# Kernel tuning notes

Hardware: AMD Instinct MI355X
Metric: run time of the kernel (lower is better)

Reference implementation:

```python
import jax, jax.numpy as jnp
import numpy as np

N_NODES = 50000
N_EDGES = 500000
D_IN, D_HID = 128, 256


def _add_self_loops(edge_index, n):
    loop = jnp.arange(n, dtype=edge_index.dtype)
    src = jnp.concatenate([edge_index[0], loop])
    dst = jnp.concatenate([edge_index[1], loop])
    return src, dst


def _gcn_layer(x, W, b, src, dst, dinv_sqrt, n):
    # x: [N, d_in] -> h: [N, d_out]
    h = x @ W
    # symmetric normalization D^{-1/2} (A+I) D^{-1/2}
    norm = dinv_sqrt[src] * dinv_sqrt[dst]          # [E+N]
    msg = h[src] * norm[:, None]                    # gather + scale
    agg = jax.ops.segment_sum(msg, dst, num_segments=n)  # scatter-add
    return agg + b


def setup_inputs() -> dict:
    key = jax.random.key(0)
    ks = jax.random.split(key, 8)
    x = jax.random.normal(ks[0], (N_NODES, D_IN), dtype=jnp.float32)
    edge_index = jax.random.randint(ks[1], (2, N_EDGES), 0, N_NODES, dtype=jnp.int64 if jax.config.read('jax_enable_x64') else jnp.int32)
    s = lambda fan_in: 1.0 / np.sqrt(fan_in)
    W1 = jax.random.uniform(ks[2], (D_IN, D_HID), jnp.float32, -s(D_IN), s(D_IN))
    b1 = jnp.zeros((D_HID,), jnp.float32)
    W2 = jax.random.uniform(ks[3], (D_HID, D_HID), jnp.float32, -s(D_HID), s(D_HID))
    b2 = jnp.zeros((D_HID,), jnp.float32)
    W3 = jax.random.uniform(ks[4], (D_HID, D_HID), jnp.float32, -s(D_HID), s(D_HID))
    b3 = jnp.zeros((D_HID,), jnp.float32)
    return {"x": x, "edge_index": edge_index, "W1": W1, "b1": b1,
            "W2": W2, "b2": b2, "W3": W3, "b3": b3}


def reference(x, edge_index, W1, b1, W2, b2, W3, b3):
    n = x.shape[0]
    src, dst = _add_self_loops(edge_index, n)
    # degree includes self loops (edge weight 1), as in torch_geometric GCNConv
    deg = jax.ops.segment_sum(jnp.ones_like(dst, dtype=x.dtype), dst, num_segments=n)
    dinv_sqrt = jnp.where(deg > 0, jax.lax.rsqrt(jnp.maximum(deg, 1e-12)), 0.0)
    h = jax.nn.relu(_gcn_layer(x, W1, b1, src, dst, dinv_sqrt, n))
    h = jax.nn.relu(_gcn_layer(h, W2, b2, src, dst, dinv_sqrt, n))
    h = _gcn_layer(h, W3, b3, src, dst, dinv_sqrt, n)
    return h
```

## Files before the change

### kernel.cpp

```cpp
#include <hip/hip_runtime.h>

#define NNODES 50000
#define NEDGES 500000
#define DIN 128
#define DHID 256
#define MPAD 50048
#define NI4 12500
#define NSB 49

typedef unsigned short u16;
typedef __attribute__((ext_vector_type(8))) _Float16 half8;
typedef __attribute__((ext_vector_type(4))) float f32x4;

__device__ __forceinline__ u16 f2h(float f) {
  union { _Float16 h; u16 u; } v; v.h = (_Float16)f; return v.u;
}
__device__ __forceinline__ float h2f(unsigned int u) {
  union { _Float16 h; u16 u; } v; v.u = (u16)u; return (float)v.h;
}

__global__ void k_zero_i32(int* __restrict__ p, int n) {
  int i = blockIdx.x * blockDim.x + threadIdx.x;
  if (i < n) p[i] = 0;
}

__global__ void k_hist(const int* __restrict__ dst, int* __restrict__ deg, int e) {
  int i = blockIdx.x * blockDim.x + threadIdx.x;
  if (i < e) atomicAdd(&deg[dst[i]], 1);
}

__global__ __launch_bounds__(256) void k_blocksum(const int* __restrict__ deg,
                                                  int* __restrict__ partials) {
  __shared__ int red[256];
  int tid = threadIdx.x;
  int t4 = blockIdx.x * 256 + tid;
  int sum = 0;
  if (t4 < NI4) {
    int4 v = ((const int4*)deg)[t4];
    sum = v.x + v.y + v.z + v.w;
  }
  red[tid] = sum;
  __syncthreads();
  for (int off = 128; off > 0; off >>= 1) {
    if (tid < off) red[tid] += red[tid + off];
    __syncthreads();
  }
  if (tid == 0) partials[blockIdx.x] = red[0];
}

__global__ __launch_bounds__(256) void k_scan2(int* __restrict__ deg,
                                               const int* __restrict__ partials,
                                               int* __restrict__ row_ptr,
                                               float* __restrict__ dinv) {
  __shared__ int sdata[256];
  __shared__ int sprefix;
  int tid = threadIdx.x, bid = blockIdx.x;
  int t4 = bid * 256 + tid;
  int4 v = make_int4(0, 0, 0, 0);
  if (t4 < NI4) v = ((const int4*)deg)[t4];
  int tsum = v.x + v.y + v.z + v.w;
  sdata[tid] = tsum;
  if (tid == 0) {
    int pre = 0;
    for (int b = 0; b < bid; ++b) pre += partials[b];
    sprefix = pre;
  }
  __syncthreads();
  for (int off = 1; off < 256; off <<= 1) {
    int val = (tid >= off) ? sdata[tid - off] : 0;
    __syncthreads();
    sdata[tid] += val;
    __syncthreads();
  }
  if (t4 < NI4) {
    int run = sdata[tid] - tsum + sprefix;
    int base = t4 * 4;
    float4 dv;
    dv.x = rsqrtf((float)v.x + 1.0f);
    dv.y = rsqrtf((float)v.y + 1.0f);
    dv.z = rsqrtf((float)v.z + 1.0f);
    dv.w = rsqrtf((float)v.w + 1.0f);
    *(float4*)(dinv + base) = dv;
    row_ptr[base + 0] = run; run += v.x;
    row_ptr[base + 1] = run; run += v.y;
    row_ptr[base + 2] = run; run += v.z;
    row_ptr[base + 3] = run; run += v.w;
    if (base + 4 == NNODES) row_ptr[NNODES] = run;
    ((int4*)deg)[t4] = make_int4(0, 0, 0, 0);
  }
}

__global__ void k_fill(const int* __restrict__ src, const int* __restrict__ dst,
                       const float* __restrict__ dinv, const int* __restrict__ row_ptr,
                       int* __restrict__ cursor, int* __restrict__ csr_src,
                       float* __restrict__ csr_nrm, int e) {
  int i = blockIdx.x * blockDim.x + threadIdx.x;
  if (i < e) {
    int d = dst[i], s = src[i];
    int pos = row_ptr[d] + atomicAdd(&cursor[d], 1);
    csr_src[pos] = s;
    csr_nrm[pos] = dinv[s] * dinv[d];
  }
}

__global__ void k_prep(const float* __restrict__ x, u16* __restrict__ xh, int total4,
                       const float* __restrict__ W1f, u16* __restrict__ P1,
                       const float* __restrict__ W2f, u16* __restrict__ P2,
                       const float* __restrict__ W3f, u16* __restrict__ P3) {
  int i = blockIdx.x * blockDim.x + threadIdx.x;
  if (i < total4) {
    float4 v = ((const float4*)x)[i];
    ushort4 o;
    o.x = f2h(v.x); o.y = f2h(v.y); o.z = f2h(v.z); o.w = f2h(v.w);
    ((ushort4*)xh)[i] = o;
  }
  const int s1 = DIN * 256, s2 = s1 + DHID * 256, s3 = s2 + DHID * 256;
  if (i < s3) {
    const float* W; u16* P; int li;
    if (i < s1)      { W = W1f; P = P1; li = i; }
    else if (i < s2) { W = W2f; P = P2; li = i - s1; }
    else             { W = W3f; P = P3; li = i - s2; }
    int k = li >> 8, n = li & 255;
    int t = k >> 5, q = (k >> 3) & 3, j = k & 7;
    int c = n >> 4, m = n & 15;
    int f = (c * 64 + q * 16 + m) * 8 + j;
    float w = W[li] * 256.0f;
    u16 hi = f2h(w);
    u16 lo = f2h(w - h2f(hi));
    P[(size_t)t * 16384 + f] = hi;
    P[(size_t)t * 16384 + 8192 + f] = lo;
  }
}

template<int K, int EPI>
__global__ __launch_bounds__(256, 6) void k_fused(const u16* __restrict__ hf,
                                                  const float* __restrict__ dinv,
                                                  const int* __restrict__ row_ptr,
                                                  const int* __restrict__ csr_src,
                                                  const float* __restrict__ csr_nrm,
                                                  const u16* __restrict__ Bpk,
                                                  const float* __restrict__ bias,
                                                  u16* __restrict__ hf16,
                                                  float* __restrict__ outf) {
  __shared__ __align__(16) u16 As[32 * K];
  __shared__ int nextrow;

  const int lane = threadIdx.x & 63;
  const int wave = threadIdx.x >> 6;

  if (threadIdx.x == 0) nextrow = 0;
  __syncthreads();

  {
    constexpr int GL = K / 8;
    const int sub = threadIdx.x % GL;
    const int gbase = lane - (lane % GL);
    const int coff = sub * 8;
    const int nbase = blockIdx.x * 32;

    for (;;) {
      int row;
      if (sub == 0) row = atomicAdd(&nextrow, 1);
      row = __shfl(row, gbase);
      if (row >= 32) break;
      const int node = nbase + row;
      float acc[8];
      if (node < NNODES) {
        float di = dinv[node];
        float s2 = di * di;
        {
          half8 v = *(const half8*)(hf + (size_t)node * K + coff);
#pragma unroll
          for (int j = 0; j < 8; ++j) acc[j] = s2 * (float)v[j];
        }
        const int p0 = row_ptr[node];
        const int p1 = row_ptr[node + 1];
        for (int e = p0; e < p1; e += 4) {
          int idx[4]; float w[4];
#pragma unroll
          for (int q = 0; q < 4; ++q) {
            int ii = (e + q < p1) ? e + q : p1 - 1;
            idx[q] = csr_src[ii];
            w[q] = (e + q < p1) ? csr_nrm[ii] : 0.0f;
          }
          half8 v[4];
#pragma unroll
          for (int q = 0; q < 4; ++q)
            v[q] = *(const half8*)(hf + (size_t)idx[q] * K + coff);
#pragma unroll
          for (int q = 0; q < 4; ++q)
#pragma unroll
            for (int j = 0; j < 8; ++j)
              acc[j] = fmaf(w[q], (float)v[q][j], acc[j]);
        }
      } else {
#pragma unroll
        for (int j = 0; j < 8; ++j) acc[j] = 0.0f;
      }
      const int wc = coff ^ ((row & 7) << 3);
      uint4 o;
      o.x = (unsigned)f2h(acc[0]) | ((unsigned)f2h(acc[1]) << 16);
      o.y = (unsigned)f2h(acc[2]) | ((unsigned)f2h(acc[3]) << 16);
      o.z = (unsigned)f2h(acc[4]) | ((unsigned)f2h(acc[5]) << 16);
      o.w = (unsigned)f2h(acc[6]) | ((unsigned)f2h(acc[7]) << 16);
      *(uint4*)&As[row * K + wc] = o;
    }
  }

  __syncthreads();

  const int cb = wave * 4;
  const int lr0 = lane & 15;
  const int lr1 = 16 + lr0;
  const int acoff = (lane >> 4) * 8;

  f32x4 acc0[4], acc1[4];
#pragma unroll
  for (int c = 0; c < 4; ++c) {
    acc0[c] = {0.f, 0.f, 0.f, 0.f};
    acc1[c] = {0.f, 0.f, 0.f, 0.f};
  }

  for (int t = 0; t < K / 32; ++t) {
    const int ac = acoff + t * 32;
    half8 a0 = *(const half8*)&As[lr0 * K + (ac ^ ((lr0 & 7) << 3))];
    half8 a1 = *(const half8*)&As[lr1 * K + (ac ^ ((lr1 & 7) << 3))];
    const u16* bt = Bpk + (size_t)t * 16384 + ((size_t)cb * 64 + lane) * 8;
#pragma unroll
    for (int c = 0; c < 4; ++c) {
      const u16* fb = bt + c * 512;
      half8 bh = *(const half8*)fb;
      half8 bl = *(const half8*)(fb + 8192);
      acc0[c] = __builtin_amdgcn_mfma_f32_16x16x32_f16(a0, bh, acc0[c], 0, 0, 0);
      acc0[c] = __builtin_amdgcn_mfma_f32_16x16x32_f16(a0, bl, acc0[c], 0, 0, 0);
      acc1[c] = __builtin_amdgcn_mfma_f32_16x16x32_f16(a1, bh, acc1[c], 0, 0, 0);
      acc1[c] = __builtin_amdgcn_mfma_f32_16x16x32_f16(a1, bl, acc1[c], 0, 0, 0);
    }
  }

  const int cbase = lane & 15;
  const int r0 = blockIdx.x * 32 + ((lane >> 4) * 4);
  const float sc = 1.0f / 256.0f;
#pragma unroll
  for (int c = 0; c < 4; ++c) {
    int col = (cb + c) * 16 + cbase;
    float bv = bias[col];
#pragma unroll
    for (int r = 0; r < 4; ++r) {
      float v0 = fmaf(acc0[c][r], sc, bv);
      float v1 = fmaf(acc1[c][r], sc, bv);
      if (EPI == 0) {
        v0 = fmaxf(v0, 0.f);
        v1 = fmaxf(v1, 0.f);
        hf16[(size_t)(r0 + r) * 256 + col] = f2h(v0);
        hf16[(size_t)(r0 + 16 + r) * 256 + col] = f2h(v1);
      } else {
        if (r0 + r < NNODES) outf[(size_t)(r0 + r) * 256 + col] = v0;
        if (r0 + 16 + r < NNODES) outf[(size_t)(r0 + 16 + r) * 256 + col] = v1;
      }
    }
  }
}

extern "C" void kernel_launch(void* const* d_in, const int* in_sizes, int n_in,
                              void* d_out, int out_size, void* d_ws, size_t ws_size,
                              hipStream_t stream) {
  const float* x  = (const float*)d_in[0];
  const int*   ei = (const int*)d_in[1];
  const float* W1 = (const float*)d_in[2];
  const float* b1 = (const float*)d_in[3];
  const float* W2 = (const float*)d_in[4];
  const float* b2 = (const float*)d_in[5];
  const float* W3 = (const float*)d_in[6];
  const float* b3 = (const float*)d_in[7];
  float* out = (float*)d_out;
  (void)in_sizes; (void)n_in; (void)out_size; (void)ws_size;

  char* ws = (char*)d_ws;
  size_t off = 0;
  auto alloc = [&](size_t bytes) -> void* {
    void* p = (void*)(ws + off);
    off += (bytes + 255) & ~(size_t)255;
    return p;
  };
  float* dinv    = (float*)alloc((size_t)NNODES * 4);
  int*   deg     = (int*)alloc((size_t)NNODES * 4);
  int*   row_ptr = (int*)alloc((size_t)(NNODES + 1) * 4);
  int*   partials= (int*)alloc((size_t)NSB * 4);
  int*   csr_src = (int*)alloc((size_t)NEDGES * 4);
  float* csr_nrm = (float*)alloc((size_t)NEDGES * 4);
  u16*   xh      = (u16*)alloc((size_t)NNODES * DIN * 2);
  u16*   hbufA   = (u16*)alloc((size_t)MPAD * 256 * 2);
  u16*   hbufB   = (u16*)alloc((size_t)MPAD * 256 * 2);
  u16*   W1pk    = (u16*)alloc((size_t)(DIN / 32) * 16384 * 2);
  u16*   W2pk    = (u16*)alloc((size_t)(DHID / 32) * 16384 * 2);
  u16*   W3pk    = (u16*)alloc((size_t)(DHID / 32) * 16384 * 2);

  const int* e_src = ei;
  const int* e_dst = ei + NEDGES;

  const int tb = 256;
  k_zero_i32<<<(NNODES + tb - 1) / tb, tb, 0, stream>>>(deg, NNODES);
  k_hist<<<(NEDGES + tb - 1) / tb, tb, 0, stream>>>(e_dst, deg, NEDGES);
  k_blocksum<<<NSB, 256, 0, stream>>>(deg, partials);
  k_scan2<<<NSB, 256, 0, stream>>>(deg, partials, row_ptr, dinv);
  k_fill<<<(NEDGES + tb - 1) / tb, tb, 0, stream>>>(e_src, e_dst, dinv, row_ptr, deg,
                                                    csr_src, csr_nrm, NEDGES);

  int x4 = NNODES * DIN / 4;
  k_prep<<<(x4 + tb - 1) / tb, tb, 0, stream>>>(x, xh, x4,
                                                W1, W1pk, W2, W2pk, W3, W3pk);

  const int gblocks = (NNODES + 31) / 32;

  k_fused<DIN, 0><<<gblocks, 256, 0, stream>>>(xh, dinv, row_ptr, csr_src, csr_nrm,
                                               W1pk, b1, hbufA, nullptr);
  k_fused<DHID, 0><<<gblocks, 256, 0, stream>>>(hbufA, dinv, row_ptr, csr_src, csr_nrm,
                                                W2pk, b2, hbufB, nullptr);
  k_fused<DHID, 1><<<gblocks, 256, 0, stream>>>(hbufB, dinv, row_ptr, csr_src, csr_nrm,
                                                W3pk, b3, nullptr, out);
}
```

Before: 305.8 us.

## Split fused GCN tile into two halves, overlapping gather with MFMA GEMM

Each 32-row block is split into two 16-row sub-tiles with separate LDS buffers. After the first half is gathered, odd waves gather the second half while even waves run the GEMM on the first half (and vice versa), so sparse gathers overlap MFMA work within a block. The zeroing kernel for degree counts is also folded into k_prep, which moves ahead of the histogram, removing one launch. The trade-off is that B fragments are loaded twice per block (once per 16-row tile) and there is an extra barrier.

```diff
diff --git a/kernel.cpp b/kernel.cpp
--- a/kernel.cpp
+++ b/kernel.cpp
@@ -17,11 +17,6 @@
 }
 __device__ __forceinline__ float h2f(unsigned int u) {
   union { _Float16 h; u16 u; } v; v.u = (u16)u; return (float)v.h;
-}
-
-__global__ void k_zero_i32(int* __restrict__ p, int n) {
-  int i = blockIdx.x * blockDim.x + threadIdx.x;
-  if (i < n) p[i] = 0;
 }
 
 __global__ void k_hist(const int* __restrict__ dst, int* __restrict__ deg, int e) {
@@ -104,10 +99,12 @@
 }
 
 __global__ void k_prep(const float* __restrict__ x, u16* __restrict__ xh, int total4,
+                       int* __restrict__ deg,
                        const float* __restrict__ W1f, u16* __restrict__ P1,
                        const float* __restrict__ W2f, u16* __restrict__ P2,
                        const float* __restrict__ W3f, u16* __restrict__ P3) {
   int i = blockIdx.x * blockDim.x + threadIdx.x;
+  if (i < NI4) ((int4*)deg)[i] = make_int4(0, 0, 0, 0);
   if (i < total4) {
     float4 v = ((const float4*)x)[i];
     ushort4 o;
@@ -142,28 +139,27 @@
                                                   const float* __restrict__ bias,
                                                   u16* __restrict__ hf16,
                                                   float* __restrict__ outf) {
-  __shared__ __align__(16) u16 As[32 * K];
-  __shared__ int nextrow;
+  __shared__ __align__(16) u16 As[2][16 * K];
+  __shared__ int nextrow[2];
 
   const int lane = threadIdx.x & 63;
   const int wave = threadIdx.x >> 6;
 
-  if (threadIdx.x == 0) nextrow = 0;
-  __syncthreads();
-
-  {
-    constexpr int GL = K / 8;
-    const int sub = threadIdx.x % GL;
-    const int gbase = lane - (lane % GL);
-    const int coff = sub * 8;
-    const int nbase = blockIdx.x * 32;
-
+  if (threadIdx.x < 2) nextrow[threadIdx.x] = 0;
+  __syncthreads();
+
+  constexpr int GL = K / 8;
+  const int sub = threadIdx.x % GL;
+  const int gbase = lane - (lane % GL);
+  const int coff = sub * 8;
+
+  auto gather_tile = [&](int tbase, int buf, int cidx) {
     for (;;) {
-      int row;
-      if (sub == 0) row = atomicAdd(&nextrow, 1);
+      int row = 0;
+      if (sub == 0) row = atomicAdd(&nextrow[cidx], 1);
       row = __shfl(row, gbase);
-      if (row >= 32) break;
-      const int node = nbase + row;
+      if (row >= 16) break;
+      const int node = tbase + row;
       float acc[8];
       if (node < NNODES) {
         float di = dinv[node];
@@ -203,63 +199,61 @@
       o.y = (unsigned)f2h(acc[2]) | ((unsigned)f2h(acc[3]) << 16);
       o.z = (unsigned)f2h(acc[4]) | ((unsigned)f2h(acc[5]) << 16);
       o.w = (unsigned)f2h(acc[6]) | ((unsigned)f2h(acc[7]) << 16);
-      *(uint4*)&As[row * K + wc] = o;
+      *(uint4*)&As[buf][row * K + wc] = o;
     }
-  }
-
-  __syncthreads();
-
-  const int cb = wave * 4;
-  const int lr0 = lane & 15;
-  const int lr1 = 16 + lr0;
-  const int acoff = (lane >> 4) * 8;
-
-  f32x4 acc0[4], acc1[4];
-#pragma unroll
-  for (int c = 0; c < 4; ++c) {
-    acc0[c] = {0.f, 0.f, 0.f, 0.f};
-    acc1[c] = {0.f, 0.f, 0.f, 0.f};
-  }
-
-  for (int t = 0; t < K / 32; ++t) {
-    const int ac = acoff + t * 32;
-    half8 a0 = *(const half8*)&As[lr0 * K + (ac ^ ((lr0 & 7) << 3))];
-    half8 a1 = *(const half8*)&As[lr1 * K + (ac ^ ((lr1 & 7) << 3))];
-    const u16* bt = Bpk + (size_t)t * 16384 + ((size_t)cb * 64 + lane) * 8;
-#pragma unroll
-    for (int c = 0; c < 4; ++c) {
-      const u16* fb = bt + c * 512;
-      half8 bh = *(const half8*)fb;
-      half8 bl = *(const half8*)(fb + 8192);
-      acc0[c] = __builtin_amdgcn_mfma_f32_16x16x32_f16(a0, bh, acc0[c], 0, 0, 0);
-      acc0[c] = __builtin_amdgcn_mfma_f32_16x16x32_f16(a0, bl, acc0[c], 0, 0, 0);
-      acc1[c] = __builtin_amdgcn_mfma_f32_16x16x32_f16(a1, bh, acc1[c], 0, 0, 0);
-      acc1[c] = __builtin_amdgcn_mfma_f32_16x16x32_f16(a1, bl, acc1[c], 0, 0, 0);
-    }
-  }
-
-  const int cbase = lane & 15;
-  const int r0 = blockIdx.x * 32 + ((lane >> 4) * 4);
-  const float sc = 1.0f / 256.0f;
-#pragma unroll
-  for (int c = 0; c < 4; ++c) {
-    int col = (cb + c) * 16 + cbase;
-    float bv = bias[col];
-#pragma unroll
-    for (int r = 0; r < 4; ++r) {
-      float v0 = fmaf(acc0[c][r], sc, bv);
-      float v1 = fmaf(acc1[c][r], sc, bv);
-      if (EPI == 0) {
-        v0 = fmaxf(v0, 0.f);
-        v1 = fmaxf(v1, 0.f);
-        hf16[(size_t)(r0 + r) * 256 + col] = f2h(v0);
-        hf16[(size_t)(r0 + 16 + r) * 256 + col] = f2h(v1);
-      } else {
-        if (r0 + r < NNODES) outf[(size_t)(r0 + r) * 256 + col] = v0;
-        if (r0 + 16 + r < NNODES) outf[(size_t)(r0 + 16 + r) * 256 + col] = v1;
+  };
+
+  auto gemm_tile = [&](int tbase, int buf) {
+    const int cb = wave * 4;
+    const int lr = lane & 15;
+    const int acoff = (lane >> 4) * 8;
+
+    f32x4 acc0[4];
+#pragma unroll
+    for (int c = 0; c < 4; ++c) acc0[c] = {0.f, 0.f, 0.f, 0.f};
+
+    for (int t = 0; t < K / 32; ++t) {
+      const int ac = acoff + t * 32;
+      half8 a0 = *(const half8*)&As[buf][lr * K + (ac ^ ((lr & 7) << 3))];
+      const u16* bt = Bpk + (size_t)t * 16384 + ((size_t)cb * 64 + lane) * 8;
+#pragma unroll
+      for (int c = 0; c < 4; ++c) {
+        const u16* fb = bt + c * 512;
+        half8 bh = *(const half8*)fb;
+        half8 bl = *(const half8*)(fb + 8192);
+        acc0[c] = __builtin_amdgcn_mfma_f32_16x16x32_f16(a0, bh, acc0[c], 0, 0, 0);
+        acc0[c] = __builtin_amdgcn_mfma_f32_16x16x32_f16(a0, bl, acc0[c], 0, 0, 0);
       }
     }
-  }
+
+    const int cbase = lane & 15;
+    const int r0 = tbase + ((lane >> 4) * 4);
+    const float sc = 1.0f / 256.0f;
+#pragma unroll
+    for (int c = 0; c < 4; ++c) {
+      int col = (cb + c) * 16 + cbase;
+      float bv = bias[col];
+#pragma unroll
+      for (int r = 0; r < 4; ++r) {
+        float v0 = fmaf(acc0[c][r], sc, bv);
+        if (EPI == 0) {
+          v0 = fmaxf(v0, 0.f);
+          hf16[(size_t)(r0 + r) * 256 + col] = f2h(v0);
+        } else {
+          if (r0 + r < NNODES) outf[(size_t)(r0 + r) * 256 + col] = v0;
+        }
+      }
+    }
+  };
+
+  const int b0 = blockIdx.x * 32;
+
+  gather_tile(b0, 0, 0);
+  __syncthreads();
+  if (wave & 1) { gather_tile(b0 + 16, 1, 1); gemm_tile(b0, 0); }
+  else          { gemm_tile(b0, 0); gather_tile(b0 + 16, 1, 1); }
+  __syncthreads();
+  gemm_tile(b0 + 16, 1);
 }
 
 extern "C" void kernel_launch(void* const* d_in, const int* in_sizes, int n_in,
@@ -300,16 +294,14 @@
   const int* e_dst = ei + NEDGES;
 
   const int tb = 256;
-  k_zero_i32<<<(NNODES + tb - 1) / tb, tb, 0, stream>>>(deg, NNODES);
+  int x4 = NNODES * DIN / 4;
+  k_prep<<<(x4 + tb - 1) / tb, tb, 0, stream>>>(x, xh, x4, deg,
+                                                W1, W1pk, W2, W2pk, W3, W3pk);
   k_hist<<<(NEDGES + tb - 1) / tb, tb, 0, stream>>>(e_dst, deg, NEDGES);
   k_blocksum<<<NSB, 256, 0, stream>>>(deg, partials);
   k_scan2<<<NSB, 256, 0, stream>>>(deg, partials, row_ptr, dinv);
   k_fill<<<(NEDGES + tb - 1) / tb, tb, 0, stream>>>(e_src, e_dst, dinv, row_ptr, deg,
                                                     csr_src, csr_nrm, NEDGES);
-
-  int x4 = NNODES * DIN / 4;
-  k_prep<<<(x4 + tb - 1) / tb, tb, 0, stream>>>(x, xh, x4,
-                                                W1, W1pk, W2, W2pk, W3, W3pk);
 
   const int gblocks = (NNODES + 31) / 32;
 
```

Measured after the change: 356.6 us. 16.6% more time.

## Merge graph preprocessing kernels into one cooperative kernel with grid syncs

Applied to the files above, without the earlier changes.

Replaces six separate preprocessing launches (zero, histogram, block sums, scan, CSR fill, fp16/weight packing) with a single cooperative kernel of 1024 blocks that uses grid.sync between phases. The goal is to remove per-launch overhead and let the x/weight conversion overlap with the degree zeroing. The cost is four grid-wide barriers, plus grid-stride loops over fewer threads, which may add serialization. Cooperative launch also requires all 1024 blocks to be co-resident.

```diff
diff --git a/kernel.cpp b/kernel.cpp
--- a/kernel.cpp
+++ b/kernel.cpp
@@ -1,4 +1,7 @@
 #include <hip/hip_runtime.h>
+#include <hip/hip_cooperative_groups.h>
+
+namespace cg = cooperative_groups;
 
 #define NNODES 50000
 #define NEDGES 500000
@@ -19,116 +22,116 @@
   union { _Float16 h; u16 u; } v; v.u = (u16)u; return (float)v.h;
 }
 
-__global__ void k_zero_i32(int* __restrict__ p, int n) {
-  int i = blockIdx.x * blockDim.x + threadIdx.x;
-  if (i < n) p[i] = 0;
-}
-
-__global__ void k_hist(const int* __restrict__ dst, int* __restrict__ deg, int e) {
-  int i = blockIdx.x * blockDim.x + threadIdx.x;
-  if (i < e) atomicAdd(&deg[dst[i]], 1);
-}
-
-__global__ __launch_bounds__(256) void k_blocksum(const int* __restrict__ deg,
-                                                  int* __restrict__ partials) {
-  __shared__ int red[256];
-  int tid = threadIdx.x;
-  int t4 = blockIdx.x * 256 + tid;
-  int sum = 0;
-  if (t4 < NI4) {
-    int4 v = ((const int4*)deg)[t4];
-    sum = v.x + v.y + v.z + v.w;
-  }
-  red[tid] = sum;
-  __syncthreads();
-  for (int off = 128; off > 0; off >>= 1) {
-    if (tid < off) red[tid] += red[tid + off];
-    __syncthreads();
-  }
-  if (tid == 0) partials[blockIdx.x] = red[0];
-}
-
-__global__ __launch_bounds__(256) void k_scan2(int* __restrict__ deg,
-                                               const int* __restrict__ partials,
-                                               int* __restrict__ row_ptr,
-                                               float* __restrict__ dinv) {
+__global__ __launch_bounds__(256, 4) void k_build(
+    const float* __restrict__ x, u16* __restrict__ xh, int total4,
+    int* __restrict__ deg,
+    const float* __restrict__ W1f, u16* __restrict__ P1,
+    const float* __restrict__ W2f, u16* __restrict__ P2,
+    const float* __restrict__ W3f, u16* __restrict__ P3,
+    const int* __restrict__ esrc, const int* __restrict__ edst,
+    int* __restrict__ row_ptr, float* __restrict__ dinv,
+    int* __restrict__ partials, int* __restrict__ csr_src,
+    float* __restrict__ csr_nrm) {
+  cg::grid_group grid = cg::this_grid();
   __shared__ int sdata[256];
   __shared__ int sprefix;
-  int tid = threadIdx.x, bid = blockIdx.x;
-  int t4 = bid * 256 + tid;
-  int4 v = make_int4(0, 0, 0, 0);
-  if (t4 < NI4) v = ((const int4*)deg)[t4];
-  int tsum = v.x + v.y + v.z + v.w;
-  sdata[tid] = tsum;
-  if (tid == 0) {
-    int pre = 0;
-    for (int b = 0; b < bid; ++b) pre += partials[b];
-    sprefix = pre;
-  }
-  __syncthreads();
-  for (int off = 1; off < 256; off <<= 1) {
-    int val = (tid >= off) ? sdata[tid - off] : 0;
-    __syncthreads();
-    sdata[tid] += val;
-    __syncthreads();
-  }
-  if (t4 < NI4) {
-    int run = sdata[tid] - tsum + sprefix;
-    int base = t4 * 4;
-    float4 dv;
-    dv.x = rsqrtf((float)v.x + 1.0f);
-    dv.y = rsqrtf((float)v.y + 1.0f);
-    dv.z = rsqrtf((float)v.z + 1.0f);
-    dv.w = rsqrtf((float)v.w + 1.0f);
-    *(float4*)(dinv + base) = dv;
-    row_ptr[base + 0] = run; run += v.x;
-    row_ptr[base + 1] = run; run += v.y;
-    row_ptr[base + 2] = run; run += v.z;
-    row_ptr[base + 3] = run; run += v.w;
-    if (base + 4 == NNODES) row_ptr[NNODES] = run;
-    ((int4*)deg)[t4] = make_int4(0, 0, 0, 0);
-  }
-}
-
-__global__ void k_fill(const int* __restrict__ src, const int* __restrict__ dst,
-                       const float* __restrict__ dinv, const int* __restrict__ row_ptr,
-                       int* __restrict__ cursor, int* __restrict__ csr_src,
-                       float* __restrict__ csr_nrm, int e) {
-  int i = blockIdx.x * blockDim.x + threadIdx.x;
-  if (i < e) {
-    int d = dst[i], s = src[i];
-    int pos = row_ptr[d] + atomicAdd(&cursor[d], 1);
-    csr_src[pos] = s;
-    csr_nrm[pos] = dinv[s] * dinv[d];
-  }
-}
-
-__global__ void k_prep(const float* __restrict__ x, u16* __restrict__ xh, int total4,
-                       const float* __restrict__ W1f, u16* __restrict__ P1,
-                       const float* __restrict__ W2f, u16* __restrict__ P2,
-                       const float* __restrict__ W3f, u16* __restrict__ P3) {
-  int i = blockIdx.x * blockDim.x + threadIdx.x;
-  if (i < total4) {
+
+  const int tid0 = blockIdx.x * blockDim.x + threadIdx.x;
+  const int gstride = gridDim.x * blockDim.x;
+
+  for (int i = tid0; i < NI4; i += gstride)
+    ((int4*)deg)[i] = make_int4(0, 0, 0, 0);
+  for (int i = tid0; i < total4; i += gstride) {
     float4 v = ((const float4*)x)[i];
     ushort4 o;
     o.x = f2h(v.x); o.y = f2h(v.y); o.z = f2h(v.z); o.w = f2h(v.w);
     ((ushort4*)xh)[i] = o;
   }
-  const int s1 = DIN * 256, s2 = s1 + DHID * 256, s3 = s2 + DHID * 256;
-  if (i < s3) {
-    const float* W; u16* P; int li;
-    if (i < s1)      { W = W1f; P = P1; li = i; }
-    else if (i < s2) { W = W2f; P = P2; li = i - s1; }
-    else             { W = W3f; P = P3; li = i - s2; }
-    int k = li >> 8, n = li & 255;
-    int t = k >> 5, q = (k >> 3) & 3, j = k & 7;
-    int c = n >> 4, m = n & 15;
-    int f = (c * 64 + q * 16 + m) * 8 + j;
-    float w = W[li] * 256.0f;
-    u16 hi = f2h(w);
-    u16 lo = f2h(w - h2f(hi));
-    P[(size_t)t * 16384 + f] = hi;
-    P[(size_t)t * 16384 + 8192 + f] = lo;
+  {
+    const int s1 = DIN * 256, s2 = s1 + DHID * 256, s3 = s2 + DHID * 256;
+    for (int i = tid0; i < s3; i += gstride) {
+      const float* W; u16* P; int li;
+      if (i < s1)      { W = W1f; P = P1; li = i; }
+      else if (i < s2) { W = W2f; P = P2; li = i - s1; }
+      else             { W = W3f; P = P3; li = i - s2; }
+      int k = li >> 8, n = li & 255;
+      int t = k >> 5, q = (k >> 3) & 3, j = k & 7;
+      int c = n >> 4, m = n & 15;
+      int f = (c * 64 + q * 16 + m) * 8 + j;
+      float w = W[li] * 256.0f;
+      u16 hi = f2h(w);
+      u16 lo = f2h(w - h2f(hi));
+      P[(size_t)t * 16384 + f] = hi;
+      P[(size_t)t * 16384 + 8192 + f] = lo;
+    }
+  }
+  grid.sync();
+
+  for (int i = tid0; i < NEDGES; i += gstride)
+    atomicAdd(&deg[edst[i]], 1);
+  grid.sync();
+
+  if (blockIdx.x < NSB) {
+    int tid = threadIdx.x;
+    int t4 = blockIdx.x * 256 + tid;
+    int sum = 0;
+    if (t4 < NI4) {
+      int4 v = ((const int4*)deg)[t4];
+      sum = v.x + v.y + v.z + v.w;
+    }
+    sdata[tid] = sum;
+    __syncthreads();
+    for (int off = 128; off > 0; off >>= 1) {
+      if (tid < off) sdata[tid] += sdata[tid + off];
+      __syncthreads();
+    }
+    if (tid == 0) partials[blockIdx.x] = sdata[0];
+  }
+  grid.sync();
+
+  if (blockIdx.x < NSB) {
+    int tid = threadIdx.x, bid = blockIdx.x;
+    int t4 = bid * 256 + tid;
+    int4 v = make_int4(0, 0, 0, 0);
+    if (t4 < NI4) v = ((const int4*)deg)[t4];
+    int tsum = v.x + v.y + v.z + v.w;
+    sdata[tid] = tsum;
+    if (tid == 0) {
+      int pre = 0;
+      for (int b = 0; b < bid; ++b) pre += partials[b];
+      sprefix = pre;
+    }
+    __syncthreads();
+    for (int off = 1; off < 256; off <<= 1) {
+      int val = (tid >= off) ? sdata[tid - off] : 0;
+      __syncthreads();
+      sdata[tid] += val;
+      __syncthreads();
+    }
+    if (t4 < NI4) {
+      int run = sdata[tid] - tsum + sprefix;
+      int base = t4 * 4;
+      float4 dv;
+      dv.x = rsqrtf((float)v.x + 1.0f);
+      dv.y = rsqrtf((float)v.y + 1.0f);
+      dv.z = rsqrtf((float)v.z + 1.0f);
+      dv.w = rsqrtf((float)v.w + 1.0f);
+      *(float4*)(dinv + base) = dv;
+      row_ptr[base + 0] = run; run += v.x;
+      row_ptr[base + 1] = run; run += v.y;
+      row_ptr[base + 2] = run; run += v.z;
+      row_ptr[base + 3] = run; run += v.w;
+      if (base + 4 == NNODES) row_ptr[NNODES] = run;
+      ((int4*)deg)[t4] = make_int4(0, 0, 0, 0);
+    }
+  }
+  grid.sync();
+
+  for (int i = tid0; i < NEDGES; i += gstride) {
+    int d = edst[i], s = esrc[i];
+    int pos = row_ptr[d] + atomicAdd(&deg[d], 1);
+    csr_src[pos] = s;
+    csr_nrm[pos] = dinv[s] * dinv[d];
   }
 }
 
@@ -159,7 +162,7 @@
     const int nbase = blockIdx.x * 32;
 
     for (;;) {
-      int row;
+      int row = 0;
       if (sub == 0) row = atomicAdd(&nextrow, 1);
       row = __shfl(row, gbase);
       if (row >= 32) break;
@@ -299,17 +302,19 @@
   const int* e_src = ei;
   const int* e_dst = ei + NEDGES;
 
-  const int tb = 256;
-  k_zero_i32<<<(NNODES + tb - 1) / tb, tb, 0, stream>>>(deg, NNODES);
-  k_hist<<<(NEDGES + tb - 1) / tb, tb, 0, stream>>>(e_dst, deg, NEDGES);
-  k_blocksum<<<NSB, 256, 0, stream>>>(deg, partials);
-  k_scan2<<<NSB, 256, 0, stream>>>(deg, partials, row_ptr, dinv);
-  k_fill<<<(NEDGES + tb - 1) / tb, tb, 0, stream>>>(e_src, e_dst, dinv, row_ptr, deg,
-                                                    csr_src, csr_nrm, NEDGES);
-
   int x4 = NNODES * DIN / 4;
-  k_prep<<<(x4 + tb - 1) / tb, tb, 0, stream>>>(x, xh, x4,
-                                                W1, W1pk, W2, W2pk, W3, W3pk);
+  {
+    void* args[] = {
+      (void*)&x, (void*)&xh, (void*)&x4, (void*)&deg,
+      (void*)&W1, (void*)&W1pk, (void*)&W2, (void*)&W2pk,
+      (void*)&W3, (void*)&W3pk,
+      (void*)&e_src, (void*)&e_dst,
+      (void*)&row_ptr, (void*)&dinv, (void*)&partials,
+      (void*)&csr_src, (void*)&csr_nrm
+    };
+    hipLaunchCooperativeKernel((void*)k_build, dim3(1024), dim3(256),
+                               args, 0, stream);
+  }
 
   const int gblocks = (NNODES + 31) / 32;
 
```

New measurement: 759.9 us. +148.5%, slower.
